# Performance work log

Measured on AMD Instinct MI355X. Metric: run time of the kernel, lower is better.

## Reference

```python
import jax, jax.numpy as jnp
import numpy as np

FILTERS = 128

def setup_inputs() -> dict:
    key = jax.random.key(0)
    ks = jax.random.split(key, 8)
    B, Nq, Nkv, C = 4, 4096, 4096, 128
    q_inputs = jax.random.normal(ks[0], (B, Nq, C), dtype=jnp.float32)
    kv_inputs = jax.random.normal(ks[1], (B, Nkv, C), dtype=jnp.float32)
    s = 1.0 / np.sqrt(C)
    Wq = jax.random.normal(ks[2], (C, FILTERS), dtype=jnp.float32) * s
    Wk = jax.random.normal(ks[3], (C, FILTERS), dtype=jnp.float32) * s
    Wv = jax.random.normal(ks[4], (C, FILTERS), dtype=jnp.float32) * s
    bq = jnp.zeros((FILTERS,), jnp.float32)
    bk = jnp.zeros((FILTERS,), jnp.float32)
    bv = jnp.zeros((FILTERS,), jnp.float32)
    return {"q_inputs": q_inputs, "kv_inputs": kv_inputs,
            "Wq": Wq, "bq": bq, "Wk": Wk, "bk": bk, "Wv": Wv, "bv": bv}

def reference(q_inputs, kv_inputs, Wq, bq, Wk, bk, Wv, bv):
    # Dense projections (last-axis matmul + bias)
    q = jnp.einsum('bnc,cf->bnf', q_inputs, Wq) + bq
    k = jnp.einsum('bmc,cf->bmf', kv_inputs, Wk) + bk
    v = jnp.einsum('bmc,cf->bmf', kv_inputs, Wv) + bv
    scale = jnp.sqrt(jnp.asarray(FILTERS, jnp.float32))
    scores = jnp.einsum('bnf,bmf->bnm', q, k) / scale  # [B, Nq, Nkv]
    weights = jax.nn.softmax(scores, axis=-1)
    return jnp.einsum('bnm,bmf->bnf', weights, v)
```

## Files before the change

### kernel.cpp

```cpp
#include <hip/hip_runtime.h>
#include <stdint.h>

typedef unsigned short u16;
typedef __bf16 bf16x8 __attribute__((ext_vector_type(8)));
typedef unsigned short u16x8 __attribute__((ext_vector_type(8)));
typedef unsigned short u16x4 __attribute__((ext_vector_type(4)));
typedef float f32x4 __attribute__((ext_vector_type(4)));

#define MFMA16(a, b, c) __builtin_amdgcn_mfma_f32_16x16x32_bf16((a), (b), (c), 0, 0, 0)

__device__ __forceinline__ u16 f2b(float f) {
    union { unsigned int i; float f; } v; v.f = f;
    unsigned int r = (v.i + 0x7FFFu + ((v.i >> 16) & 1u)) >> 16;
    return (u16)r;
}

constexpr int N = 4096;
constexpr int Cc = 128;
constexpr int Fc = 128;
constexpr int BATCH = 4;

constexpr int XS_STRIDE = 136;
constexpr int WT_STRIDE = 136;
constexpr int KS_STRIDE = 136;
constexpr int VTS_STRIDE = 136;
constexpr int PS_STRIDE = 72;

__global__ __launch_bounds__(256) void wtrans_kernel(
    const float* __restrict__ Wq, const float* __restrict__ Wk,
    const float* __restrict__ Wv, u16* __restrict__ WtG)
{
    __shared__ __align__(16) u16 Wl[128 * 132];
    const int tid = threadIdx.x;
    const int which = blockIdx.x;
    const float* W = which == 0 ? Wq : (which == 1 ? Wk : Wv);
#pragma unroll
    for (int it = 0; it < 16; ++it) {
        int idx4 = tid + it * 256; int e0 = idx4 * 4;
        int c = e0 >> 7, f = e0 & 127;
        float4 wv = *(const float4*)(W + e0);
        u16x4 h; h[0] = f2b(wv.x); h[1] = f2b(wv.y); h[2] = f2b(wv.z); h[3] = f2b(wv.w);
        *(u16x4*)&Wl[c * 132 + f] = h;
    }
    __syncthreads();
    u16* out = WtG + which * 16384;
#pragma unroll
    for (int it = 0; it < 8; ++it) {
        int idx8 = tid + it * 256; int e0 = idx8 * 8;
        int f = e0 >> 7, c = e0 & 127;
        u16x8 h;
#pragma unroll
        for (int j = 0; j < 8; ++j) h[j] = Wl[(c + j) * 132 + f];
        *(u16x8*)(out + e0) = h;
    }
}

__global__ __launch_bounds__(256) void proj_kernel(
    const float* __restrict__ q_in, const float* __restrict__ kv_in,
    const u16* __restrict__ WtG,
    const float* __restrict__ bq, const float* __restrict__ bk,
    const float* __restrict__ bv,
    u16* __restrict__ Qw, u16* __restrict__ Kw, u16* __restrict__ Vtw)
{
    __shared__ __align__(16) u16 Xs[64 * XS_STRIDE];
    __shared__ __align__(16) u16 Wt[128 * WT_STRIDE];

    const int tid = threadIdx.x;
    const int which = blockIdx.y;
    const int b = blockIdx.z;
    const int m0 = blockIdx.x * 64;

    const float* X = (which == 0 ? q_in : kv_in) + ((size_t)b * N + m0) * Cc;
    const u16* Wsrc = WtG + which * 16384;
    const float* bias = which == 0 ? bq : (which == 1 ? bk : bv);

#pragma unroll
    for (int it = 0; it < 8; ++it) {
        int idx4 = tid + it * 256; int e0 = idx4 * 4;
        int r = e0 >> 7, c = e0 & 127;
        float4 xv = *(const float4*)(X + e0);
        u16x4 h; h[0] = f2b(xv.x); h[1] = f2b(xv.y); h[2] = f2b(xv.z); h[3] = f2b(xv.w);
        *(u16x4*)&Xs[r * XS_STRIDE + c] = h;
    }
#pragma unroll
    for (int it = 0; it < 8; ++it) {
        int idx8 = tid + it * 256; int e0 = idx8 * 8;
        int f = e0 >> 7, c = e0 & 127;
        *(u16x8*)&Wt[f * WT_STRIDE + c] = *(const u16x8*)(Wsrc + e0);
    }
    __syncthreads();

    const int lane = tid & 63;
    const int w = tid >> 6;
    const int n16 = lane & 15;
    const int quad = lane >> 4;

    if (which < 2) {
        bf16x8 ax[4];
#pragma unroll
        for (int kk = 0; kk < 4; ++kk)
            ax[kk] = *(const bf16x8*)&Xs[(w * 16 + n16) * XS_STRIDE + kk * 32 + quad * 8];
        const float scale = (which == 0) ? 0.08838834764831845f : 1.0f;
        u16* Out = (which == 0) ? Qw : Kw;
#pragma unroll
        for (int ft = 0; ft < 8; ++ft) {
            f32x4 acc = {0.f, 0.f, 0.f, 0.f};
#pragma unroll
            for (int kk = 0; kk < 4; ++kk) {
                bf16x8 bw = *(const bf16x8*)&Wt[(ft * 16 + n16) * WT_STRIDE + kk * 32 + quad * 8];
                acc = MFMA16(ax[kk], bw, acc);
            }
            float bias_f = bias[ft * 16 + n16];
#pragma unroll
            for (int r = 0; r < 4; ++r) {
                int row = m0 + w * 16 + quad * 4 + r;
                Out[((size_t)b * N + row) * Fc + ft * 16 + n16] = f2b((acc[r] + bias_f) * scale);
            }
        }
    } else {
#pragma unroll
        for (int ft2 = 0; ft2 < 2; ++ft2) {
            int ftg = w * 2 + ft2;
            bf16x8 aw[4];
#pragma unroll
            for (int kk = 0; kk < 4; ++kk)
                aw[kk] = *(const bf16x8*)&Wt[(ftg * 16 + n16) * WT_STRIDE + kk * 32 + quad * 8];
            float bias4[4];
#pragma unroll
            for (int r = 0; r < 4; ++r) bias4[r] = bias[ftg * 16 + quad * 4 + r];
#pragma unroll
            for (int nt = 0; nt < 4; ++nt) {
                f32x4 acc = {0.f, 0.f, 0.f, 0.f};
#pragma unroll
                for (int kk = 0; kk < 4; ++kk) {
                    bf16x8 bx = *(const bf16x8*)&Xs[(nt * 16 + n16) * XS_STRIDE + kk * 32 + quad * 8];
                    acc = MFMA16(aw[kk], bx, acc);
                }
#pragma unroll
                for (int r = 0; r < 4; ++r) {
                    int fg = ftg * 16 + quad * 4 + r;
                    int rowg = m0 + nt * 16 + n16;
                    Vtw[((size_t)b * Fc + fg) * N + rowg] = f2b(acc[r] + bias4[r]);
                }
            }
        }
    }
}

__global__ __launch_bounds__(512, 2) void attn_kernel(
    const u16* __restrict__ Qw, const u16* __restrict__ Kw,
    const u16* __restrict__ Vtw, float* __restrict__ out)
{
    __shared__ __align__(16) u16 Ks[128 * KS_STRIDE];
    __shared__ __align__(16) u16 Vts[128 * VTS_STRIDE];
    __shared__ __align__(16) u16 Ps[8 * 16 * PS_STRIDE];

    const int tid = threadIdx.x;
    const int b = blockIdx.y;
    const int q0 = blockIdx.x * 64;
    const int lane = tid & 63;
    const int w = tid >> 6;
    const int wq = w & 3;
    const int grp = w >> 2;
    const int n16 = lane & 15;
    const int quad = lane >> 4;

    bf16x8 aq[4];
    {
        const u16* qrow = Qw + ((size_t)b * N + q0 + wq * 16 + n16) * Cc;
#pragma unroll
        for (int kk = 0; kk < 4; ++kk)
            aq[kk] = *(const bf16x8*)(qrow + kk * 32 + quad * 8);
    }

    int rr[4], cc[4];
#pragma unroll
    for (int it = 0; it < 4; ++it) {
        int idx8 = tid + it * 512; int e0 = idx8 * 8;
        rr[it] = e0 >> 7; cc[it] = e0 & 127;
    }
    const u16* Kbase = Kw + (size_t)b * N * Cc;
    const u16* Vbase = Vtw + (size_t)b * Fc * N;

    u16x8 kreg[4], vreg[4];
#pragma unroll
    for (int it = 0; it < 4; ++it) {
        kreg[it] = *(const u16x8*)(Kbase + (size_t)rr[it] * Cc + cc[it]);
        vreg[it] = *(const u16x8*)(Vbase + (size_t)rr[it] * N + cc[it]);
    }

    f32x4 o[8];
#pragma unroll
    for (int ct = 0; ct < 8; ++ct) o[ct] = (f32x4){0.f, 0.f, 0.f, 0.f};
    float lloc = 0.f;

    u16* Psw = &Ps[w * 16 * PS_STRIDE];

    for (int t = 0; t < N / 128; ++t) {
#pragma unroll
        for (int it = 0; it < 4; ++it) {
            *(u16x8*)&Ks[rr[it] * KS_STRIDE + cc[it]] = kreg[it];
            *(u16x8*)&Vts[rr[it] * VTS_STRIDE + cc[it]] = vreg[it];
        }
        __syncthreads();

        if (t + 1 < N / 128) {
            int k0n = (t + 1) * 128;
#pragma unroll
            for (int it = 0; it < 4; ++it) {
                kreg[it] = *(const u16x8*)(Kbase + (size_t)(k0n + rr[it]) * Cc + cc[it]);
                vreg[it] = *(const u16x8*)(Vbase + (size_t)rr[it] * N + k0n + cc[it]);
            }
        }

        f32x4 st[4];
#pragma unroll
        for (int kt = 0; kt < 4; ++kt) {
            f32x4 acc = {0.f, 0.f, 0.f, 0.f};
#pragma unroll
            for (int kk = 0; kk < 4; ++kk) {
                bf16x8 ak = *(const bf16x8*)&Ks[(grp * 64 + kt * 16 + n16) * KS_STRIDE + kk * 32 + quad * 8];
                acc = MFMA16(ak, aq[kk], acc);
            }
            st[kt] = acc;
        }

#pragma unroll
        for (int kt = 0; kt < 4; ++kt) {
            float e0 = __expf(st[kt][0]), e1 = __expf(st[kt][1]);
            float e2 = __expf(st[kt][2]), e3 = __expf(st[kt][3]);
            lloc += (e0 + e1) + (e2 + e3);
            u16x4 pk; pk[0] = f2b(e0); pk[1] = f2b(e1); pk[2] = f2b(e2); pk[3] = f2b(e3);
            *(u16x4*)&Psw[n16 * PS_STRIDE + kt * 16 + quad * 4] = pk;
        }

        bf16x8 pa[2];
#pragma unroll
        for (int kch = 0; kch < 2; ++kch)
            pa[kch] = *(const bf16x8*)&Psw[n16 * PS_STRIDE + kch * 32 + quad * 8];
#pragma unroll
        for (int ct = 0; ct < 8; ++ct) {
#pragma unroll
            for (int kch = 0; kch < 2; ++kch) {
                bf16x8 bv_ = *(const bf16x8*)&Vts[(ct * 16 + n16) * VTS_STRIDE + grp * 64 + kch * 32 + quad * 8];
                o[ct] = MFMA16(pa[kch], bv_, o[ct]);
            }
        }
        __syncthreads();
    }

    float lv = lloc;
    lv += __shfl_xor(lv, 16);
    lv += __shfl_xor(lv, 32);

    float* Om = (float*)&Ks[0];
    float* Lm = (float*)&Vts[0];
    if (grp == 1) {
#pragma unroll
        for (int ct = 0; ct < 8; ++ct)
#pragma unroll
            for (int r = 0; r < 4; ++r)
                Om[(wq * 16 + quad * 4 + r) * 132 + ct * 16 + n16] = o[ct][r];
        if (lane < 16) Lm[wq * 16 + n16] = lv;
    }
    __syncthreads();
    if (grp == 0) {
        float lsum[4];
#pragma unroll
        for (int r = 0; r < 4; ++r)
            lsum[r] = __shfl(lv, quad * 4 + r) + Lm[wq * 16 + quad * 4 + r];
#pragma unroll
        for (int ct = 0; ct < 8; ++ct) {
#pragma unroll
            for (int r = 0; r < 4; ++r) {
                int q = q0 + wq * 16 + quad * 4 + r;
                float ov = o[ct][r] + Om[(wq * 16 + quad * 4 + r) * 132 + ct * 16 + n16];
                out[((size_t)b * N + q) * Fc + ct * 16 + n16] = ov / lsum[r];
            }
        }
    }
}

extern "C" void kernel_launch(void* const* d_in, const int* in_sizes, int n_in,
                              void* d_out, int out_size, void* d_ws, size_t ws_size,
                              hipStream_t stream) {
    (void)in_sizes; (void)n_in; (void)out_size; (void)ws_size;
    const float* q_in  = (const float*)d_in[0];
    const float* kv_in = (const float*)d_in[1];
    const float* Wq = (const float*)d_in[2];
    const float* bq = (const float*)d_in[3];
    const float* Wk = (const float*)d_in[4];
    const float* bk = (const float*)d_in[5];
    const float* Wv = (const float*)d_in[6];
    const float* bv = (const float*)d_in[7];

    const size_t qkv = (size_t)BATCH * N * Fc;
    u16* Qw  = (u16*)d_ws;
    u16* Kw  = Qw + qkv;
    u16* Vtw = Kw + qkv;
    u16* WtG = Vtw + qkv;

    wtrans_kernel<<<dim3(3), dim3(256), 0, stream>>>(Wq, Wk, Wv, WtG);
    proj_kernel<<<dim3(64, 3, BATCH), dim3(256), 0, stream>>>(
        q_in, kv_in, WtG, bq, bk, bv, Qw, Kw, Vtw);
    attn_kernel<<<dim3(64, BATCH), dim3(512), 0, stream>>>(
        Qw, Kw, Vtw, (float*)d_out);
}
```

Before: 145.2 us.

## Repartition attention waves into 2 query groups by 4 key groups

Each wave now handles a 32-query by 32-key tile instead of a 16-query by 64-key tile. Every K fragment and V fragment loaded from LDS now feeds two MFMAs (one per query subtile), which cuts LDS read traffic per MFMA. The price is a 4-way instead of 2-way cross-wave reduction of the output and row sums, done through a larger shared scratch region overlaid on the K/V buffers. Doubling the output accumulators per wave also raises register pressure under the existing launch bounds, which could cause spilling.

```diff
diff --git a/kernel.cpp b/kernel.cpp
--- a/kernel.cpp
+++ b/kernel.cpp
@@ -24,7 +24,8 @@
 constexpr int WT_STRIDE = 136;
 constexpr int KS_STRIDE = 136;
 constexpr int VTS_STRIDE = 136;
-constexpr int PS_STRIDE = 72;
+constexpr int PS_STRIDE = 40;
+constexpr int OM_STRIDE = 132;
 
 __global__ __launch_bounds__(256) void wtrans_kernel(
     const float* __restrict__ Wq, const float* __restrict__ Wk,
@@ -151,26 +152,30 @@
     const u16* __restrict__ Qw, const u16* __restrict__ Kw,
     const u16* __restrict__ Vtw, float* __restrict__ out)
 {
-    __shared__ __align__(16) u16 Ks[128 * KS_STRIDE];
-    __shared__ __align__(16) u16 Vts[128 * VTS_STRIDE];
-    __shared__ __align__(16) u16 Ps[8 * 16 * PS_STRIDE];
+    __shared__ __align__(16) char smem_raw[102400];
+    u16* Ks  = (u16*)smem_raw;
+    u16* Vts = Ks + 128 * KS_STRIDE;
+    u16* Ps  = Vts + 128 * VTS_STRIDE;
+    float* Om = (float*)smem_raw;
+    float* Lm = Om + 6 * 32 * OM_STRIDE;
 
     const int tid = threadIdx.x;
     const int b = blockIdx.y;
     const int q0 = blockIdx.x * 64;
     const int lane = tid & 63;
     const int w = tid >> 6;
-    const int wq = w & 3;
-    const int grp = w >> 2;
+    const int kg = w & 3;
+    const int qg = w >> 2;
     const int n16 = lane & 15;
     const int quad = lane >> 4;
 
-    bf16x8 aq[4];
-    {
-        const u16* qrow = Qw + ((size_t)b * N + q0 + wq * 16 + n16) * Cc;
+    bf16x8 aq[2][4];
+#pragma unroll
+    for (int qs = 0; qs < 2; ++qs) {
+        const u16* qrow = Qw + ((size_t)b * N + q0 + qg * 32 + qs * 16 + n16) * Cc;
 #pragma unroll
         for (int kk = 0; kk < 4; ++kk)
-            aq[kk] = *(const bf16x8*)(qrow + kk * 32 + quad * 8);
+            aq[qs][kk] = *(const bf16x8*)(qrow + kk * 32 + quad * 8);
     }
 
     int rr[4], cc[4];
@@ -189,12 +194,14 @@
         vreg[it] = *(const u16x8*)(Vbase + (size_t)rr[it] * N + cc[it]);
     }
 
-    f32x4 o[8];
-#pragma unroll
-    for (int ct = 0; ct < 8; ++ct) o[ct] = (f32x4){0.f, 0.f, 0.f, 0.f};
-    float lloc = 0.f;
-
-    u16* Psw = &Ps[w * 16 * PS_STRIDE];
+    f32x4 o[2][8];
+#pragma unroll
+    for (int qs = 0; qs < 2; ++qs)
+#pragma unroll
+        for (int ct = 0; ct < 8; ++ct) o[qs][ct] = (f32x4){0.f, 0.f, 0.f, 0.f};
+    float lloc[2] = {0.f, 0.f};
+
+    u16* Psw = Ps + w * 32 * PS_STRIDE;
 
     for (int t = 0; t < N / 128; ++t) {
 #pragma unroll
@@ -213,69 +220,93 @@
             }
         }
 
-        f32x4 st[4];
-#pragma unroll
-        for (int kt = 0; kt < 4; ++kt) {
-            f32x4 acc = {0.f, 0.f, 0.f, 0.f};
-#pragma unroll
-            for (int kk = 0; kk < 4; ++kk) {
-                bf16x8 ak = *(const bf16x8*)&Ks[(grp * 64 + kt * 16 + n16) * KS_STRIDE + kk * 32 + quad * 8];
-                acc = MFMA16(ak, aq[kk], acc);
-            }
-            st[kt] = acc;
-        }
-
-#pragma unroll
-        for (int kt = 0; kt < 4; ++kt) {
-            float e0 = __expf(st[kt][0]), e1 = __expf(st[kt][1]);
-            float e2 = __expf(st[kt][2]), e3 = __expf(st[kt][3]);
-            lloc += (e0 + e1) + (e2 + e3);
-            u16x4 pk; pk[0] = f2b(e0); pk[1] = f2b(e1); pk[2] = f2b(e2); pk[3] = f2b(e3);
-            *(u16x4*)&Psw[n16 * PS_STRIDE + kt * 16 + quad * 4] = pk;
-        }
+        bf16x8 ak[2][4];
+#pragma unroll
+        for (int ks = 0; ks < 2; ++ks)
+#pragma unroll
+            for (int kk = 0; kk < 4; ++kk)
+                ak[ks][kk] = *(const bf16x8*)&Ks[(kg * 32 + ks * 16 + n16) * KS_STRIDE + kk * 32 + quad * 8];
+
+        f32x4 st[2][2];
+#pragma unroll
+        for (int qs = 0; qs < 2; ++qs)
+#pragma unroll
+            for (int ks = 0; ks < 2; ++ks) {
+                f32x4 acc = {0.f, 0.f, 0.f, 0.f};
+#pragma unroll
+                for (int kk = 0; kk < 4; ++kk)
+                    acc = MFMA16(ak[ks][kk], aq[qs][kk], acc);
+                st[qs][ks] = acc;
+            }
+
+#pragma unroll
+        for (int qs = 0; qs < 2; ++qs)
+#pragma unroll
+            for (int ks = 0; ks < 2; ++ks) {
+                float e0 = __expf(st[qs][ks][0]), e1 = __expf(st[qs][ks][1]);
+                float e2 = __expf(st[qs][ks][2]), e3 = __expf(st[qs][ks][3]);
+                lloc[qs] += (e0 + e1) + (e2 + e3);
+                u16x4 pk; pk[0] = f2b(e0); pk[1] = f2b(e1); pk[2] = f2b(e2); pk[3] = f2b(e3);
+                *(u16x4*)&Psw[(qs * 16 + n16) * PS_STRIDE + ks * 16 + quad * 4] = pk;
+            }
 
         bf16x8 pa[2];
 #pragma unroll
-        for (int kch = 0; kch < 2; ++kch)
-            pa[kch] = *(const bf16x8*)&Psw[n16 * PS_STRIDE + kch * 32 + quad * 8];
+        for (int qs = 0; qs < 2; ++qs)
+            pa[qs] = *(const bf16x8*)&Psw[(qs * 16 + n16) * PS_STRIDE + quad * 8];
 #pragma unroll
         for (int ct = 0; ct < 8; ++ct) {
-#pragma unroll
-            for (int kch = 0; kch < 2; ++kch) {
-                bf16x8 bv_ = *(const bf16x8*)&Vts[(ct * 16 + n16) * VTS_STRIDE + grp * 64 + kch * 32 + quad * 8];
-                o[ct] = MFMA16(pa[kch], bv_, o[ct]);
-            }
+            bf16x8 bv_ = *(const bf16x8*)&Vts[(ct * 16 + n16) * VTS_STRIDE + kg * 32 + quad * 8];
+            o[0][ct] = MFMA16(pa[0], bv_, o[0][ct]);
+            o[1][ct] = MFMA16(pa[1], bv_, o[1][ct]);
         }
         __syncthreads();
     }
 
-    float lv = lloc;
-    lv += __shfl_xor(lv, 16);
-    lv += __shfl_xor(lv, 32);
-
-    float* Om = (float*)&Ks[0];
-    float* Lm = (float*)&Vts[0];
-    if (grp == 1) {
-#pragma unroll
-        for (int ct = 0; ct < 8; ++ct)
-#pragma unroll
-            for (int r = 0; r < 4; ++r)
-                Om[(wq * 16 + quad * 4 + r) * 132 + ct * 16 + n16] = o[ct][r];
-        if (lane < 16) Lm[wq * 16 + n16] = lv;
+    float lv[2];
+#pragma unroll
+    for (int qs = 0; qs < 2; ++qs) {
+        float v = lloc[qs];
+        v += __shfl_xor(v, 16);
+        v += __shfl_xor(v, 32);
+        lv[qs] = v;
+    }
+
+    if (kg != 0) {
+#pragma unroll
+        for (int qs = 0; qs < 2; ++qs) {
+#pragma unroll
+            for (int ct = 0; ct < 8; ++ct)
+#pragma unroll
+                for (int r = 0; r < 4; ++r)
+                    Om[((size_t)((kg - 1) * 2 + qg) * 32 + qs * 16 + quad * 4 + r) * OM_STRIDE + ct * 16 + n16] = o[qs][ct][r];
+            if (quad == 0) Lm[(kg - 1) * 64 + qg * 32 + qs * 16 + n16] = lv[qs];
+        }
     }
     __syncthreads();
-    if (grp == 0) {
-        float lsum[4];
-#pragma unroll
-        for (int r = 0; r < 4; ++r)
-            lsum[r] = __shfl(lv, quad * 4 + r) + Lm[wq * 16 + quad * 4 + r];
-#pragma unroll
-        for (int ct = 0; ct < 8; ++ct) {
+    if (kg == 0) {
+#pragma unroll
+        for (int qs = 0; qs < 2; ++qs) {
+            float lsum[4];
 #pragma unroll
             for (int r = 0; r < 4; ++r) {
-                int q = q0 + wq * 16 + quad * 4 + r;
-                float ov = o[ct][r] + Om[(wq * 16 + quad * 4 + r) * 132 + ct * 16 + n16];
-                out[((size_t)b * N + q) * Fc + ct * 16 + n16] = ov / lsum[r];
+                float s = __shfl(lv[qs], quad * 4 + r);
+#pragma unroll
+                for (int j = 0; j < 3; ++j)
+                    s += Lm[j * 64 + qg * 32 + qs * 16 + quad * 4 + r];
+                lsum[r] = s;
+            }
+#pragma unroll
+            for (int ct = 0; ct < 8; ++ct) {
+#pragma unroll
+                for (int r = 0; r < 4; ++r) {
+                    float ov = o[qs][ct][r];
+#pragma unroll
+                    for (int j = 0; j < 3; ++j)
+                        ov += Om[((size_t)(j * 2 + qg) * 32 + qs * 16 + quad * 4 + r) * OM_STRIDE + ct * 16 + n16];
+                    int q = q0 + qg * 32 + qs * 16 + quad * 4 + r;
+                    out[((size_t)b * N + q) * Fc + ct * 16 + n16] = ov / lsum[r];
+                }
             }
         }
     }
```

Result: faster. 139.0 us (-4.3%).

## Split attention keys four ways per block, pass P through lane shuffles

Applied to the files above, without the earlier changes.

The attention kernel now handles 32 queries per block (256 blocks, not 128) and splits each 128-key tile across four wave groups of 32 keys, not two of 64. The P matrix moves from the score MFMA output layout to the PV A-operand layout through lane shuffles, so the per-wave LDS scratch buffer and its write/read round trip are gone. Launch bounds ask for 4 blocks per CU, and LDS is shared between the K/V tiles and the final reduction. The aim is more blocks to fill the CUs and less LDS traffic. In exchange, each block streams the full K/V for only half as many queries, which doubles K/V loads in total, and the final reduction across the key splits is larger. The non-max-subtracted exp softmax is kept from before.

```diff
diff --git a/kernel.cpp b/kernel.cpp
--- a/kernel.cpp
+++ b/kernel.cpp
@@ -24,7 +24,6 @@
 constexpr int WT_STRIDE = 136;
 constexpr int KS_STRIDE = 136;
 constexpr int VTS_STRIDE = 136;
-constexpr int PS_STRIDE = 72;
 
 __global__ __launch_bounds__(256) void wtrans_kernel(
     const float* __restrict__ Wq, const float* __restrict__ Wk,
@@ -147,46 +146,43 @@
     }
 }
 
-__global__ __launch_bounds__(512, 2) void attn_kernel(
+__global__ __launch_bounds__(512, 4) void attn_kernel(
     const u16* __restrict__ Qw, const u16* __restrict__ Kw,
     const u16* __restrict__ Vtw, float* __restrict__ out)
 {
-    __shared__ __align__(16) u16 Ks[128 * KS_STRIDE];
-    __shared__ __align__(16) u16 Vts[128 * VTS_STRIDE];
-    __shared__ __align__(16) u16 Ps[8 * 16 * PS_STRIDE];
+    __shared__ __align__(16) char smem[(128 * KS_STRIDE + 128 * VTS_STRIDE) * 2];
+    u16* Ks  = (u16*)smem;
+    u16* Vts = Ks + 128 * KS_STRIDE;
+    float* Om = (float*)smem;
+    float* Lm = Om + 96 * 132;
 
     const int tid = threadIdx.x;
     const int b = blockIdx.y;
-    const int q0 = blockIdx.x * 64;
+    const int q0 = blockIdx.x * 32;
     const int lane = tid & 63;
     const int w = tid >> 6;
-    const int wq = w & 3;
-    const int grp = w >> 2;
+    const int kg = w & 3;
+    const int qg = w >> 2;
     const int n16 = lane & 15;
     const int quad = lane >> 4;
 
     bf16x8 aq[4];
     {
-        const u16* qrow = Qw + ((size_t)b * N + q0 + wq * 16 + n16) * Cc;
+        const u16* qrow = Qw + ((size_t)b * N + q0 + qg * 16 + n16) * Cc;
 #pragma unroll
         for (int kk = 0; kk < 4; ++kk)
             aq[kk] = *(const bf16x8*)(qrow + kk * 32 + quad * 8);
     }
 
-    int rr[4], cc[4];
+    const u16* Kbase = Kw + (size_t)b * N * Cc;
+    const u16* Vbase = Vtw + (size_t)b * Fc * N;
+
+    u16x8 kreg[4], vreg[4];
 #pragma unroll
     for (int it = 0; it < 4; ++it) {
         int idx8 = tid + it * 512; int e0 = idx8 * 8;
-        rr[it] = e0 >> 7; cc[it] = e0 & 127;
-    }
-    const u16* Kbase = Kw + (size_t)b * N * Cc;
-    const u16* Vbase = Vtw + (size_t)b * Fc * N;
-
-    u16x8 kreg[4], vreg[4];
-#pragma unroll
-    for (int it = 0; it < 4; ++it) {
-        kreg[it] = *(const u16x8*)(Kbase + (size_t)rr[it] * Cc + cc[it]);
-        vreg[it] = *(const u16x8*)(Vbase + (size_t)rr[it] * N + cc[it]);
+        kreg[it] = *(const u16x8*)(Kbase + (size_t)(e0 >> 7) * Cc + (e0 & 127));
+        vreg[it] = *(const u16x8*)(Vbase + (size_t)(idx8 >> 4) * N + (idx8 & 15) * 8);
     }
 
     f32x4 o[8];
@@ -194,57 +190,61 @@
     for (int ct = 0; ct < 8; ++ct) o[ct] = (f32x4){0.f, 0.f, 0.f, 0.f};
     float lloc = 0.f;
 
-    u16* Psw = &Ps[w * 16 * PS_STRIDE];
-
     for (int t = 0; t < N / 128; ++t) {
 #pragma unroll
         for (int it = 0; it < 4; ++it) {
-            *(u16x8*)&Ks[rr[it] * KS_STRIDE + cc[it]] = kreg[it];
-            *(u16x8*)&Vts[rr[it] * VTS_STRIDE + cc[it]] = vreg[it];
+            int idx8 = tid + it * 512; int e0 = idx8 * 8;
+            *(u16x8*)&Ks[(e0 >> 7) * KS_STRIDE + (e0 & 127)] = kreg[it];
+            *(u16x8*)&Vts[(idx8 >> 4) * VTS_STRIDE + (idx8 & 15) * 8] = vreg[it];
         }
         __syncthreads();
+
+        f32x4 st[2];
+#pragma unroll
+        for (int ks = 0; ks < 2; ++ks) {
+            f32x4 acc = {0.f, 0.f, 0.f, 0.f};
+#pragma unroll
+            for (int kk = 0; kk < 4; ++kk) {
+                bf16x8 ak = *(const bf16x8*)&Ks[(kg * 32 + ks * 16 + n16) * KS_STRIDE + kk * 32 + quad * 8];
+                acc = MFMA16(ak, aq[kk], acc);
+            }
+            st[ks] = acc;
+        }
 
         if (t + 1 < N / 128) {
             int k0n = (t + 1) * 128;
 #pragma unroll
             for (int it = 0; it < 4; ++it) {
-                kreg[it] = *(const u16x8*)(Kbase + (size_t)(k0n + rr[it]) * Cc + cc[it]);
-                vreg[it] = *(const u16x8*)(Vbase + (size_t)rr[it] * N + k0n + cc[it]);
-            }
-        }
-
-        f32x4 st[4];
-#pragma unroll
-        for (int kt = 0; kt < 4; ++kt) {
-            f32x4 acc = {0.f, 0.f, 0.f, 0.f};
-#pragma unroll
-            for (int kk = 0; kk < 4; ++kk) {
-                bf16x8 ak = *(const bf16x8*)&Ks[(grp * 64 + kt * 16 + n16) * KS_STRIDE + kk * 32 + quad * 8];
-                acc = MFMA16(ak, aq[kk], acc);
-            }
-            st[kt] = acc;
-        }
-
-#pragma unroll
-        for (int kt = 0; kt < 4; ++kt) {
-            float e0 = __expf(st[kt][0]), e1 = __expf(st[kt][1]);
-            float e2 = __expf(st[kt][2]), e3 = __expf(st[kt][3]);
-            lloc += (e0 + e1) + (e2 + e3);
-            u16x4 pk; pk[0] = f2b(e0); pk[1] = f2b(e1); pk[2] = f2b(e2); pk[3] = f2b(e3);
-            *(u16x4*)&Psw[n16 * PS_STRIDE + kt * 16 + quad * 4] = pk;
-        }
-
-        bf16x8 pa[2];
-#pragma unroll
-        for (int kch = 0; kch < 2; ++kch)
-            pa[kch] = *(const bf16x8*)&Psw[n16 * PS_STRIDE + kch * 32 + quad * 8];
+                int idx8 = tid + it * 512; int e0 = idx8 * 8;
+                kreg[it] = *(const u16x8*)(Kbase + (size_t)(k0n + (e0 >> 7)) * Cc + (e0 & 127));
+                vreg[it] = *(const u16x8*)(Vbase + (size_t)(idx8 >> 4) * N + k0n + (idx8 & 15) * 8);
+            }
+        }
+
+        bf16x8 pa;
+        {
+            unsigned int packed[4];
+#pragma unroll
+            for (int r = 0; r < 4; ++r) {
+                float e0 = __expf(st[0][r]);
+                float e1 = __expf(st[1][r]);
+                lloc += e0 + e1;
+                packed[r] = (unsigned int)f2b(e0) | ((unsigned int)f2b(e1) << 16);
+            }
+            const int sbase = n16 + ((quad & 1) << 5);
+            union { bf16x8 v; u16x8 h; } pk;
+#pragma unroll
+            for (int j = 0; j < 8; ++j) {
+                unsigned int pv = (unsigned int)__shfl((int)packed[j & 3], sbase + ((j >> 2) << 4));
+                pk.h[j] = (quad < 2) ? (u16)(pv & 0xFFFFu) : (u16)(pv >> 16);
+            }
+            pa = pk.v;
+        }
+
 #pragma unroll
         for (int ct = 0; ct < 8; ++ct) {
-#pragma unroll
-            for (int kch = 0; kch < 2; ++kch) {
-                bf16x8 bv_ = *(const bf16x8*)&Vts[(ct * 16 + n16) * VTS_STRIDE + grp * 64 + kch * 32 + quad * 8];
-                o[ct] = MFMA16(pa[kch], bv_, o[ct]);
-            }
+            bf16x8 bv_ = *(const bf16x8*)&Vts[(ct * 16 + n16) * VTS_STRIDE + kg * 32 + quad * 8];
+            o[ct] = MFMA16(pa, bv_, o[ct]);
         }
         __syncthreads();
     }
@@ -253,28 +253,35 @@
     lv += __shfl_xor(lv, 16);
     lv += __shfl_xor(lv, 32);
 
-    float* Om = (float*)&Ks[0];
-    float* Lm = (float*)&Vts[0];
-    if (grp == 1) {
+    if (kg != 0) {
+        int rbase = (kg - 1) * 32 + qg * 16;
 #pragma unroll
         for (int ct = 0; ct < 8; ++ct)
 #pragma unroll
             for (int r = 0; r < 4; ++r)
-                Om[(wq * 16 + quad * 4 + r) * 132 + ct * 16 + n16] = o[ct][r];
-        if (lane < 16) Lm[wq * 16 + n16] = lv;
+                Om[(rbase + quad * 4 + r) * 132 + ct * 16 + n16] = o[ct][r];
+        if (quad == 0) Lm[rbase + n16] = lv;
     }
     __syncthreads();
-    if (grp == 0) {
+    if (kg == 0) {
         float lsum[4];
 #pragma unroll
-        for (int r = 0; r < 4; ++r)
-            lsum[r] = __shfl(lv, quad * 4 + r) + Lm[wq * 16 + quad * 4 + r];
+        for (int r = 0; r < 4; ++r) {
+            float s = __shfl(lv, quad * 4 + r);
+#pragma unroll
+            for (int j = 0; j < 3; ++j)
+                s += Lm[j * 32 + qg * 16 + quad * 4 + r];
+            lsum[r] = s;
+        }
 #pragma unroll
         for (int ct = 0; ct < 8; ++ct) {
 #pragma unroll
             for (int r = 0; r < 4; ++r) {
-                int q = q0 + wq * 16 + quad * 4 + r;
-                float ov = o[ct][r] + Om[(wq * 16 + quad * 4 + r) * 132 + ct * 16 + n16];
+                float ov = o[ct][r];
+#pragma unroll
+                for (int j = 0; j < 3; ++j)
+                    ov += Om[(j * 32 + qg * 16 + quad * 4 + r) * 132 + ct * 16 + n16];
+                int q = q0 + qg * 16 + quad * 4 + r;
                 out[((size_t)b * N + q) * Fc + ct * 16 + n16] = ov / lsum[r];
             }
         }
@@ -303,6 +310,6 @@
     wtrans_kernel<<<dim3(3), dim3(256), 0, stream>>>(Wq, Wk, Wv, WtG);
     proj_kernel<<<dim3(64, 3, BATCH), dim3(256), 0, stream>>>(
         q_in, kv_in, WtG, bq, bk, bv, Qw, Kw, Vtw);
-    attn_kernel<<<dim3(64, BATCH), dim3(512), 0, stream>>>(
+    attn_kernel<<<dim3(128, BATCH), dim3(512), 0, stream>>>(
         Qw, Kw, Vtw, (float*)d_out);
 }
```

Measured after the change: 164.7 us. +13.4%, slower.
